# Performance work log

Measured on AMD Instinct MI355X. Metric: run time of the kernel, lower is better.

## Reference

```python
import jax, jax.numpy as jnp
import numpy as np

B, T, D = 32, 1024, 1024
N, L = 256, 768
H = 16
TE = 2048


def layernorm(x, g, b, eps=1e-5):
    m = jnp.mean(x, axis=-1, keepdims=True)
    v = jnp.var(x, axis=-1, keepdims=True)
    return (x - m) * jax.lax.rsqrt(v + eps) * g + b


def setup_inputs() -> dict:
    key = jax.random.key(0)
    ks = jax.random.split(key, 16)
    s = 0.02
    return {
        "x": jax.random.normal(ks[0], (B, T, D), jnp.float32),
        "xf": jax.random.normal(ks[1], (B, N, L), jnp.float32),
        "emb": jax.random.normal(ks[2], (B, TE), jnp.float32),
        "src_mask": jnp.ones((B, T, 1), jnp.float32),
        "cond_type": jax.random.randint(ks[3], (B, 1, 1), 0, 100),
        # LayerNorm params
        "ln_x_g": jnp.ones((D,), jnp.float32), "ln_x_b": jnp.zeros((D,), jnp.float32),
        "ln_t_g": jnp.ones((L,), jnp.float32), "ln_t_b": jnp.zeros((L,), jnp.float32),
        # Q/K/V projections
        "Wq": jax.random.normal(ks[4], (D, D), jnp.float32) * s, "bq": jnp.zeros((D,), jnp.float32),
        "Wk": jax.random.normal(ks[5], (L, D), jnp.float32) * s, "bk": jnp.zeros((D,), jnp.float32),
        "Wv": jax.random.normal(ks[6], (L, D), jnp.float32) * s, "bv": jnp.zeros((D,), jnp.float32),
        # StylizationBlock: SiLU -> Linear(TE, 2D); LayerNorm(D); SiLU -> Linear(D, D)
        "We": jax.random.normal(ks[7], (TE, 2 * D), jnp.float32) * s, "be": jnp.zeros((2 * D,), jnp.float32),
        "ln_y_g": jnp.ones((D,), jnp.float32), "ln_y_b": jnp.zeros((D,), jnp.float32),
        "Wo": jax.random.normal(ks[8], (D, D), jnp.float32) * s, "bo": jnp.zeros((D,), jnp.float32),
    }


def reference(x, xf, emb, src_mask, cond_type,
              ln_x_g, ln_x_b, ln_t_g, ln_t_b,
              Wq, bq, Wk, bk, Wv, bv,
              We, be, ln_y_g, ln_y_b, Wo, bo):
    Bh, Th, Dh = x.shape
    Nn = xf.shape[1]
    head = Dh // H

    # text condition gate: (B,1,1), constant per batch element
    tcond = (cond_type % 10 > 0).astype(x.dtype).reshape(Bh, 1, 1)

    q = (layernorm(x, ln_x_g, ln_x_b) @ Wq + bq).reshape(Bh, Th, H, head)
    xf_n = layernorm(xf, ln_t_g, ln_t_b)
    k = (xf_n @ Wk + bk).reshape(Bh, Nn, H, head)

    # B,T,N,H scores (note: no 1/sqrt(d) scaling, as in the original)
    att = jnp.einsum('bthd,bnhd->btnh', q, k)
    att = att + (1.0 - tcond.reshape(Bh, 1, 1, 1)) * -1000000.0
    att = jax.nn.softmax(att, axis=2)

    v = ((xf_n @ Wv + bv) * tcond).reshape(Bh, Nn, H, head)
    y = jnp.einsum('btnh,bnhd->bthd', att, v).reshape(Bh, Th, Dh)

    # StylizationBlock (dropout inactive in eval)
    emb_out = jax.nn.silu(emb) @ We + be            # B, 2D
    scale, shift = jnp.split(emb_out, 2, axis=-1)   # B, D each
    h = layernorm(y, ln_y_g, ln_y_b) * (1.0 + scale[:, None, :]) + shift[:, None, :]
    h = jax.nn.silu(h) @ Wo + bo
    return x + h
```

## Files before the change

### kernel.cpp

```cpp
#include <hip/hip_runtime.h>
#include <hip/hip_bf16.h>

#define DEV __device__ __forceinline__

typedef __attribute__((ext_vector_type(8))) short bf16x8;
typedef __attribute__((ext_vector_type(4))) float f32x4;
typedef __attribute__((ext_vector_type(8))) unsigned short u16x8;

DEV unsigned short f2bf(float f){
  unsigned int b = __float_as_uint(f);
  return (unsigned short)((b + 0x7fffu + ((b >> 16) & 1u)) >> 16);
}
DEV float bf2f(unsigned short u){ return __uint_as_float(((unsigned int)u)<<16); }

DEV float silu_f(float v){ return v / (1.f + __expf(-v)); }

DEV void gl_lds16(const void* g, void* l){
  __builtin_amdgcn_global_load_lds((const __attribute__((address_space(1))) void*)g,
                                   (__attribute__((address_space(3))) void*)l, 16, 0, 0);
}

__global__ __launch_bounds__(256) void ln_rows(const float* __restrict__ x,
    const float* __restrict__ g, const float* __restrict__ bt,
    unsigned short* __restrict__ out, int D, int nvec)
{
  int row = blockIdx.x, t = threadIdx.x;
  const float4* xr = (const float4*)(x + (size_t)row * D);
  float4 v = make_float4(0.f,0.f,0.f,0.f);
  if (t < nvec) v = xr[t];
  float s  = v.x+v.y+v.z+v.w;
  float s2 = v.x*v.x+v.y*v.y+v.z*v.z+v.w*v.w;
  #pragma unroll
  for (int o=32;o;o>>=1){ s += __shfl_down(s,o,64); s2 += __shfl_down(s2,o,64); }
  __shared__ float red[8];
  if ((t&63)==0){ red[t>>6]=s; red[4+(t>>6)]=s2; }
  __syncthreads();
  float fs  = red[0]+red[1]+red[2]+red[3];
  float fs2 = red[4]+red[5]+red[6]+red[7];
  float mean = fs / (float)D;
  float var  = fmaxf(fs2/(float)D - mean*mean, 0.f);
  float rstd = rsqrtf(var + 1e-5f);
  if (t < nvec){
    float4 gv = ((const float4*)g)[t];
    float4 bv = ((const float4*)bt)[t];
    ushort4 o4;
    o4.x = f2bf((v.x-mean)*rstd*gv.x + bv.x);
    o4.y = f2bf((v.y-mean)*rstd*gv.y + bv.y);
    o4.z = f2bf((v.z-mean)*rstd*gv.z + bv.z);
    o4.w = f2bf((v.w-mean)*rstd*gv.w + bv.w);
    *(ushort4*)(out + (size_t)row*D + t*4) = o4;
  }
}

__global__ __launch_bounds__(256) void wconv(const float* __restrict__ W,
    unsigned short* __restrict__ Wt, int K, int N)
{
  __shared__ float tile[32][33];
  int n0 = blockIdx.x<<5, k0 = blockIdx.y<<5;
  int tx = threadIdx.x & 31, ty = threadIdx.x >> 5;
  #pragma unroll
  for (int i=0;i<4;i++)
    tile[ty + i*8][tx] = W[(size_t)(k0 + ty + i*8)*N + n0 + tx];
  __syncthreads();
  #pragma unroll
  for (int i=0;i<4;i++)
    Wt[(size_t)(n0 + ty + i*8)*K + k0 + tx] = f2bf(tile[tx][ty + i*8]);
}

__global__ __launch_bounds__(256) void bcat(const float* __restrict__ a,
    const float* __restrict__ b, float* __restrict__ o)
{
  int i = blockIdx.x*256 + threadIdx.x;
  o[i] = (i < 1024) ? a[i] : b[i-1024];
}

template<int EPI>
__global__ __launch_bounds__(256,4) void gemm128(
  const unsigned char* __restrict__ A, const unsigned char* __restrict__ Wt,
  const float* __restrict__ bias, void* __restrict__ Cout,
  const float* __restrict__ Xadd, int M, int N, int K, int gxshift)
{
  __shared__ __align__(16) unsigned char lds[32768];
  const int nwg = gridDim.x;
  const int chunk = nwg >> 3;
  const int wg = blockIdx.x;
  const int lg = (wg & 7) * chunk + (wg >> 3);
  const int bx = lg & ((1<<gxshift)-1);
  const int by = lg >> gxshift;
  const int tid = threadIdx.x, w = tid>>6, lane = tid&63;
  const int l15 = lane&15, lq = lane>>4;
  const int m0 = by<<7, n0 = bx<<7;
  const size_t K2 = (size_t)K<<1;
  const int KT = K>>6;
  const int wr = (w>>1)&1, wc = w&1;
  const int srow = lane>>3;
  const int scb  = (lane&7)<<4;

  f32x4 acc[4][4];
  f32x4 zero = {0.f,0.f,0.f,0.f};
  #pragma unroll
  for (int i=0;i<4;i++)
    #pragma unroll
    for (int j=0;j<4;j++) acc[i][j] = zero;

  auto stage = [&](int kt){
    const size_t kb = (size_t)kt<<7;
    #pragma unroll
    for (int inst=0; inst<4; ++inst){
      int base = w*1024 + inst*4096;
      int row  = (base>>7) + srow;
      int cs   = scb ^ ((row&7)<<4);
      gl_lds16(A  + (size_t)(m0+row)*K2 + kb + cs, lds + base);
      gl_lds16(Wt + (size_t)(n0+row)*K2 + kb + cs, lds + 16384 + base);
    }
  };

  for (int kt=0; kt<KT; ++kt){
    stage(kt);
    __syncthreads();
    const unsigned char* ldsA = lds;
    const unsigned char* ldsB = lds + 16384;
    bf16x8 af[2][4], bfr[2][4];
    #pragma unroll
    for (int i=0;i<4;i++){
      int r = wr*64 + i*16 + l15;
      int rb = r<<7, sw = (r&7)<<4;
      af[0][i] = *(const bf16x8*)(ldsA + rb + ((lq*16) ^ sw));
      af[1][i] = *(const bf16x8*)(ldsA + rb + ((64 + lq*16) ^ sw));
    }
    #pragma unroll
    for (int j=0;j<4;j++){
      int r = wc*64 + j*16 + l15;
      int rb = r<<7, sw = (r&7)<<4;
      bfr[0][j] = *(const bf16x8*)(ldsB + rb + ((lq*16) ^ sw));
      bfr[1][j] = *(const bf16x8*)(ldsB + rb + ((64 + lq*16) ^ sw));
    }
    #pragma unroll
    for (int kc=0;kc<2;kc++)
      #pragma unroll
      for (int i=0;i<4;i++)
        #pragma unroll
        for (int j=0;j<4;j++)
          acc[i][j] = __builtin_amdgcn_mfma_f32_16x16x32_bf16(af[kc][i], bfr[kc][j], acc[i][j], 0,0,0);
    __syncthreads();
  }
  #pragma unroll
  for (int j=0;j<4;j++){
    int n = n0 + wc*64 + j*16 + l15;
    float bv = bias[n];
    #pragma unroll
    for (int i=0;i<4;i++){
      int mb = m0 + wr*64 + i*16 + lq*4;
      #pragma unroll
      for (int r=0;r<4;r++){
        size_t idx = (size_t)(mb+r)*N + n;
        float val = acc[i][j][r] + bv;
        if (EPI==0) ((unsigned short*)Cout)[idx] = f2bf(val);
        else        ((float*)Cout)[idx] = Xadd[idx] + val;
      }
    }
  }
}

__global__ __launch_bounds__(256) void vtransp(const unsigned short* __restrict__ v,
                                               int vstride, unsigned char* __restrict__ vt)
{
  __shared__ __align__(16) unsigned short tile[16384];
  int h = blockIdx.x, b = blockIdx.y, tid = threadIdx.x;
  const unsigned short* src = v + (size_t)b*256*vstride + h*64;
  #pragma unroll
  for (int it=0; it<8; ++it){
    int idx = it*256 + tid;
    int n = idx>>3, dc = idx&7;
    *(f32x4*)&tile[n*64 + dc*8] = *(const f32x4*)(src + (size_t)n*vstride + dc*8);
  }
  __syncthreads();
  unsigned char* dst = vt + (size_t)(b*16+h)*32768;
  #pragma unroll
  for (int it=0; it<8; ++it){
    int idx = it*256 + tid;
    int d = idx>>5, nc = idx&31;
    u16x8 o;
    #pragma unroll
    for (int j=0;j<8;j++) o[j] = tile[(nc*8+j)*64 + d];
    *(u16x8*)(dst + d*512 + ((nc*16) ^ ((d&7)<<4))) = o;
  }
}

__global__ __launch_bounds__(256,2) void attn64(
  const unsigned char* __restrict__ qg, const unsigned char* __restrict__ kg,
  int kstride, const unsigned char* __restrict__ vtg, const int* __restrict__ cond,
  unsigned short* __restrict__ yout)
{
  __shared__ __align__(16) unsigned char lds[73728];
  const int wg = blockIdx.x;
  const int lg = (wg & 7) * 1024 + (wg >> 3);
  const int t0 = (lg & 15) * 64;
  const int h  = (lg >> 4) & 15;
  const int b  = lg >> 8;
  const int tid = threadIdx.x, w = tid>>6, lane = tid&63;
  const int l15 = lane&15, lq = lane>>4;

  const unsigned char* kbase = kg + (size_t)b*256*kstride + (size_t)h*128;
  const unsigned char* vtb   = vtg + (size_t)(b*16+h)*32768;
  #pragma unroll
  for (int i=0;i<8;i++){
    int base = (w*8+i)*1024;
    int n  = (base>>7) + (lane>>3);
    int cb = (lane&7)<<4;
    gl_lds16(kbase + (size_t)n*kstride + (cb ^ ((n&7)<<4)), lds + base);
    gl_lds16(vtb + base + lane*16, lds + 32768 + base);
  }
  const unsigned char* qbase = qg + (size_t)(b*1024 + t0)*2048 + h*128;
  #pragma unroll
  for (int i=0;i<2;i++){
    int row = i*32 + (tid>>3);
    int cs  = ((tid&7)<<4) ^ ((row&7)<<4);
    gl_lds16(qbase + (size_t)row*2048 + cs, lds + 65536 + i*4096 + w*1024);
  }
  __syncthreads();

  const int qr = w*16 + l15;
  const int qsw = (qr&7)<<4;
  bf16x8 aq0 = *(const bf16x8*)(lds + 65536 + qr*128 + ((lq*16) ^ qsw));
  bf16x8 aq1 = *(const bf16x8*)(lds + 65536 + qr*128 + ((64 + lq*16) ^ qsw));

  f32x4 zero = {0.f,0.f,0.f,0.f};
  f32x4 s[16];
  #pragma unroll
  for (int nt=0;nt<16;nt++) s[nt] = zero;
  #pragma unroll
  for (int nt=0;nt<16;nt++){
    int n = nt*16 + l15;
    int rb = n<<7, sw = (n&7)<<4;
    bf16x8 kb0 = *(const bf16x8*)(lds + rb + ((lq*16) ^ sw));
    bf16x8 kb1 = *(const bf16x8*)(lds + rb + ((64 + lq*16) ^ sw));
    s[nt] = __builtin_amdgcn_mfma_f32_16x16x32_bf16(aq0, kb0, s[nt], 0,0,0);
    s[nt] = __builtin_amdgcn_mfma_f32_16x16x32_bf16(aq1, kb1, s[nt], 0,0,0);
  }
  #pragma unroll
  for (int r=0;r<4;r++){
    float m = s[0][r];
    #pragma unroll
    for (int nt=1;nt<16;nt++) m = fmaxf(m, s[nt][r]);
    m = fmaxf(m, __shfl_xor(m,1,64));
    m = fmaxf(m, __shfl_xor(m,2,64));
    m = fmaxf(m, __shfl_xor(m,4,64));
    m = fmaxf(m, __shfl_xor(m,8,64));
    float sum = 0.f;
    #pragma unroll
    for (int nt=0;nt<16;nt++){ float p = __expf(s[nt][r]-m); s[nt][r]=p; sum+=p; }
    sum += __shfl_xor(sum,1,64);
    sum += __shfl_xor(sum,2,64);
    sum += __shfl_xor(sum,4,64);
    sum += __shfl_xor(sum,8,64);
    float inv = 1.f/sum;
    #pragma unroll
    for (int nt=0;nt<16;nt++) s[nt][r] *= inv;
  }
  __syncthreads();
  #pragma unroll
  for (int nt=0;nt<16;nt++){
    int n = nt*16 + l15;
    int nb = (n>>3)<<4, nr = (n&7)<<1;
    #pragma unroll
    for (int r=0;r<4;r++){
      int tl = w*16 + lq*4 + r;
      *(unsigned short*)(lds + tl*512 + ((nb ^ ((tl&7)<<4)) | nr)) = f2bf(s[nt][r]);
    }
  }
  __syncthreads();
  f32x4 yv[4];
  #pragma unroll
  for (int dt=0;dt<4;dt++) yv[dt] = zero;
  const int tl = w*16 + l15;
  const int swp = (tl&7)<<4;
  #pragma unroll
  for (int kc=0;kc<8;kc++){
    bf16x8 pa = *(const bf16x8*)(lds + tl*512 + ((kc*64 + lq*16) ^ swp));
    #pragma unroll
    for (int dt=0;dt<4;dt++){
      int d = dt*16 + l15;
      bf16x8 vbv = *(const bf16x8*)(lds + 32768 + d*512 + ((kc*64 + lq*16) ^ ((d&7)<<4)));
      yv[dt] = __builtin_amdgcn_mfma_f32_16x16x32_bf16(pa, vbv, yv[dt], 0,0,0);
    }
  }
  float tc = (cond[b] % 10 > 0) ? 1.f : 0.f;
  #pragma unroll
  for (int dt=0;dt<4;dt++){
    #pragma unroll
    for (int r=0;r<4;r++){
      int tt = t0 + w*16 + lq*4 + r;
      yout[(size_t)(b*1024 + tt)*1024 + h*64 + dt*16 + l15] = f2bf(yv[dt][r]*tc);
    }
  }
}

__global__ __launch_bounds__(256) void embgemm(const float* __restrict__ emb,
    const float* __restrict__ We, float* __restrict__ epart)
{
  __shared__ float a[32][128];
  int cb = blockIdx.x, ks = blockIdx.y, tid = threadIdx.x;
  int k0 = ks<<7;
  #pragma unroll
  for (int it=0; it<4; ++it){
    int fi = it*256 + tid;
    int r = fi>>5, c4 = (fi&31)<<2;
    float4 vv = *(const float4*)(emb + (size_t)r*2048 + k0 + c4);
    vv.x = silu_f(vv.x); vv.y = silu_f(vv.y); vv.z = silu_f(vv.z); vv.w = silu_f(vv.w);
    *(float4*)&a[r][c4] = vv;
  }
  __syncthreads();
  int c0 = (cb<<8) + tid;
  float acc[32];
  #pragma unroll
  for (int r=0;r<32;r++) acc[r]=0.f;
  for (int kk=0;kk<128;kk++){
    float wv = We[(size_t)(k0+kk)*2048 + c0];
    #pragma unroll
    for (int r=0;r<32;r++) acc[r] += a[r][kk]*wv;
  }
  #pragma unroll
  for (int r=0;r<32;r++) epart[(size_t)(ks*32 + r)*2048 + c0] = acc[r];
}

__global__ __launch_bounds__(256) void embred(const float* __restrict__ epart,
    const float* __restrict__ be, float* __restrict__ eo)
{
  int idx = blockIdx.x*256 + threadIdx.x;
  float s = be[idx & 2047];
  #pragma unroll
  for (int ks=0;ks<16;ks++) s += epart[(size_t)ks*65536 + idx];
  eo[idx] = s;
}

__global__ __launch_bounds__(256) void styl(const unsigned short* __restrict__ y,
    const float* __restrict__ g, const float* __restrict__ bt,
    const float* __restrict__ eo, unsigned short* __restrict__ hout)
{
  int row = blockIdx.x, t = threadIdx.x, b = row>>10;
  ushort4 yv4 = ((const ushort4*)(y + (size_t)row*1024))[t];
  float in[4] = {bf2f(yv4.x), bf2f(yv4.y), bf2f(yv4.z), bf2f(yv4.w)};
  float s  = in[0]+in[1]+in[2]+in[3];
  float s2 = in[0]*in[0]+in[1]*in[1]+in[2]*in[2]+in[3]*in[3];
  #pragma unroll
  for (int o=32;o;o>>=1){ s += __shfl_down(s,o,64); s2 += __shfl_down(s2,o,64); }
  __shared__ float red[8];
  if ((t&63)==0){ red[t>>6]=s; red[4+(t>>6)]=s2; }
  __syncthreads();
  float fs  = red[0]+red[1]+red[2]+red[3];
  float fs2 = red[4]+red[5]+red[6]+red[7];
  float mean = fs*(1.f/1024.f);
  float var  = fmaxf(fs2*(1.f/1024.f) - mean*mean, 0.f);
  float rstd = rsqrtf(var + 1e-5f);
  float4 gv = ((const float4*)g)[t];
  float4 bv = ((const float4*)bt)[t];
  float4 sc = ((const float4*)(eo + (size_t)b*2048))[t];
  float4 sh = ((const float4*)(eo + (size_t)b*2048 + 1024))[t];
  float gg[4]  = {gv.x,gv.y,gv.z,gv.w};
  float bb[4]  = {bv.x,bv.y,bv.z,bv.w};
  float scs[4] = {sc.x,sc.y,sc.z,sc.w};
  float shs[4] = {sh.x,sh.y,sh.z,sh.w};
  unsigned short oo[4];
  #pragma unroll
  for (int c=0;c<4;c++){
    float hv = (in[c]-mean)*rstd*gg[c] + bb[c];
    hv = hv*(1.f+scs[c]) + shs[c];
    oo[c] = f2bf(silu_f(hv));
  }
  ushort4 o4; o4.x=oo[0]; o4.y=oo[1]; o4.z=oo[2]; o4.w=oo[3];
  *(ushort4*)(hout + (size_t)row*1024 + t*4) = o4;
}

extern "C" void kernel_launch(void* const* d_in, const int* in_sizes, int n_in,
                              void* d_out, int out_size, void* d_ws, size_t ws_size,
                              hipStream_t stream) {
  const float* x      = (const float*)d_in[0];
  const float* xf     = (const float*)d_in[1];
  const float* emb    = (const float*)d_in[2];
  const int*   cond   = (const int*)d_in[4];
  const float* ln_x_g = (const float*)d_in[5];
  const float* ln_x_b = (const float*)d_in[6];
  const float* ln_t_g = (const float*)d_in[7];
  const float* ln_t_b = (const float*)d_in[8];
  const float* Wq     = (const float*)d_in[9];
  const float* bq     = (const float*)d_in[10];
  const float* Wk     = (const float*)d_in[11];
  const float* bk     = (const float*)d_in[12];
  const float* Wv     = (const float*)d_in[13];
  const float* bv     = (const float*)d_in[14];
  const float* We     = (const float*)d_in[15];
  const float* be     = (const float*)d_in[16];
  const float* ln_y_g = (const float*)d_in[17];
  const float* ln_y_b = (const float*)d_in[18];
  const float* Wo     = (const float*)d_in[19];
  const float* bo     = (const float*)d_in[20];
  float* out = (float*)d_out;

  unsigned char* ws = (unsigned char*)d_ws;
  size_t off = 0;
  auto take = [&](size_t n){ unsigned char* p = ws + off; off += (n + 255) & ~(size_t)255; return p; };
  unsigned char* r1   = take(67108864);
  unsigned char* qb   = take(67108864);
  unsigned char* xfn  = take(12582912);
  unsigned char* kvb  = take(33554432);
  unsigned char* vtb  = take(16777216);
  unsigned char* wqt  = take(2097152);
  unsigned char* wkvt = take(3145728);
  unsigned char* wot  = take(2097152);
  unsigned char* eo   = take(262144);
  unsigned char* bkv  = take(8192);
  float* epart = (float*)r1;

  dim3 blk(256);
  wconv<<<dim3(32,32), blk, 0, stream>>>(Wq, (unsigned short*)wqt, 1024, 1024);
  wconv<<<dim3(32,24), blk, 0, stream>>>(Wk, (unsigned short*)wkvt,  768, 1024);
  wconv<<<dim3(32,24), blk, 0, stream>>>(Wv, (unsigned short*)wkvt + (size_t)1024*768, 768, 1024);
  wconv<<<dim3(32,32), blk, 0, stream>>>(Wo, (unsigned short*)wot, 1024, 1024);
  bcat<<<8, blk, 0, stream>>>(bk, bv, (float*)bkv);
  ln_rows<<<32768, blk, 0, stream>>>(x,  ln_x_g, ln_x_b, (unsigned short*)r1,  1024, 256);
  ln_rows<<<8192,  blk, 0, stream>>>(xf, ln_t_g, ln_t_b, (unsigned short*)xfn,  768, 192);
  gemm128<0><<<2048, blk, 0, stream>>>(r1,  wqt,  bq, qb, nullptr, 32768, 1024, 1024, 3);
  gemm128<0><<<1024, blk, 0, stream>>>(xfn, wkvt, (const float*)bkv, kvb, nullptr, 8192, 2048, 768, 4);
  vtransp<<<dim3(16,32), blk, 0, stream>>>((const unsigned short*)kvb + 1024, 2048, vtb);
  embgemm<<<dim3(8,16), blk, 0, stream>>>(emb, We, epart);
  embred<<<256, blk, 0, stream>>>(epart, be, (float*)eo);
  attn64<<<8192, blk, 0, stream>>>(qb, kvb, 4096, vtb, cond, (unsigned short*)qb);
  styl<<<32768, blk, 0, stream>>>((const unsigned short*)qb, ln_y_g, ln_y_b, (const float*)eo, (unsigned short*)r1);
  gemm128<1><<<2048, blk, 0, stream>>>(r1, wot, bo, out, x, 32768, 1024, 1024, 3);
}
```

Baseline: 487.0 us.

## Replace 128x128 GEMM with 256x256 double-buffered, phase-interleaved 8-wave GEMM

Replaces the 128x128 single-buffered GEMM with a 256x256 tile kernel using 512 threads and two 64KB LDS buffers. Global-to-LDS loads for the next two k-steps are issued between four MFMA phases, with barriers and setprio around each phase. The goal is to hide global load latency and raise arithmetic intensity per LDS byte for the Q, KV and output projections. The cost is 128KB of LDS per block, which limits occupancy. The hand-tuned vmcnt waits are fragile and must match the order of the issued loads.

```diff
diff --git a/kernel.cpp b/kernel.cpp
--- a/kernel.cpp
+++ b/kernel.cpp
@@ -74,13 +74,26 @@
   o[i] = (i < 1024) ? a[i] : b[i-1024];
 }
 
+template<int MH, int KS>
+DEV void phase_mfma(f32x4 (&acc)[8][4], const bf16x8 (&aF)[4], const bf16x8 (&bB)[2][4]){
+  __builtin_amdgcn_s_barrier();
+  __builtin_amdgcn_s_setprio(1);
+  #pragma unroll
+  for (int i=0;i<4;i++)
+    #pragma unroll
+    for (int j=0;j<4;j++)
+      acc[MH*4+i][j] = __builtin_amdgcn_mfma_f32_16x16x32_bf16(aF[i], bB[KS][j], acc[MH*4+i][j], 0,0,0);
+  __builtin_amdgcn_s_setprio(0);
+  __builtin_amdgcn_s_barrier();
+}
+
 template<int EPI>
-__global__ __launch_bounds__(256,4) void gemm128(
+__global__ __launch_bounds__(512,2) void gemm256(
   const unsigned char* __restrict__ A, const unsigned char* __restrict__ Wt,
   const float* __restrict__ bias, void* __restrict__ Cout,
   const float* __restrict__ Xadd, int M, int N, int K, int gxshift)
 {
-  __shared__ __align__(16) unsigned char lds[32768];
+  __shared__ __align__(16) unsigned char lds[131072];
   const int nwg = gridDim.x;
   const int chunk = nwg >> 3;
   const int wg = blockIdx.x;
@@ -89,72 +102,85 @@
   const int by = lg >> gxshift;
   const int tid = threadIdx.x, w = tid>>6, lane = tid&63;
   const int l15 = lane&15, lq = lane>>4;
-  const int m0 = by<<7, n0 = bx<<7;
+  const int wr = w>>2, wc = w&3;
+  const int m0 = by<<8, n0 = bx<<8;
   const size_t K2 = (size_t)K<<1;
-  const int KT = K>>6;
-  const int wr = (w>>1)&1, wc = w&1;
-  const int srow = lane>>3;
-  const int scb  = (lane&7)<<4;
-
-  f32x4 acc[4][4];
+  const int NT = K>>6;
+
+  const int srow = w*8 + (lane>>3);
+  const int scs  = (((lane&7) ^ (lane>>3))<<4);
+
+  f32x4 acc[8][4];
   f32x4 zero = {0.f,0.f,0.f,0.f};
   #pragma unroll
-  for (int i=0;i<4;i++)
+  for (int i=0;i<8;i++)
     #pragma unroll
     for (int j=0;j<4;j++) acc[i][j] = zero;
 
-  auto stage = [&](int kt){
-    const size_t kb = (size_t)kt<<7;
-    #pragma unroll
-    for (int inst=0; inst<4; ++inst){
-      int base = w*1024 + inst*4096;
-      int row  = (base>>7) + srow;
-      int cs   = scb ^ ((row&7)<<4);
-      gl_lds16(A  + (size_t)(m0+row)*K2 + kb + cs, lds + base);
-      gl_lds16(Wt + (size_t)(n0+row)*K2 + kb + cs, lds + 16384 + base);
-    }
+  auto stg = [&](int bf, int mat, int c, int t){
+    const unsigned char* src = mat ? Wt : A;
+    int prow = mat ? n0 : m0;
+    gl_lds16(src + (size_t)(prow + c*64 + srow)*K2 + ((size_t)t<<7) + scs,
+             lds + bf*65536 + mat*32768 + c*8192 + w*1024);
   };
-
-  for (int kt=0; kt<KT; ++kt){
-    stage(kt);
-    __syncthreads();
-    const unsigned char* ldsA = lds;
-    const unsigned char* ldsB = lds + 16384;
-    bf16x8 af[2][4], bfr[2][4];
-    #pragma unroll
-    for (int i=0;i<4;i++){
-      int r = wr*64 + i*16 + l15;
-      int rb = r<<7, sw = (r&7)<<4;
-      af[0][i] = *(const bf16x8*)(ldsA + rb + ((lq*16) ^ sw));
-      af[1][i] = *(const bf16x8*)(ldsA + rb + ((64 + lq*16) ^ sw));
-    }
-    #pragma unroll
-    for (int j=0;j<4;j++){
-      int r = wc*64 + j*16 + l15;
-      int rb = r<<7, sw = (r&7)<<4;
-      bfr[0][j] = *(const bf16x8*)(ldsB + rb + ((lq*16) ^ sw));
-      bfr[1][j] = *(const bf16x8*)(ldsB + rb + ((64 + lq*16) ^ sw));
-    }
-    #pragma unroll
-    for (int kc=0;kc<2;kc++)
-      #pragma unroll
-      for (int i=0;i<4;i++)
-        #pragma unroll
-        for (int j=0;j<4;j++)
-          acc[i][j] = __builtin_amdgcn_mfma_f32_16x16x32_bf16(af[kc][i], bfr[kc][j], acc[i][j], 0,0,0);
-    __syncthreads();
-  }
+  auto ldA = [&](int mh, int i, int ks, int bf)->bf16x8 {
+    int r = wr*128 + mh*64 + i*16 + l15;
+    return *(const bf16x8*)(lds + bf*65536 + r*128 + ((ks*64 + lq*16) ^ ((r&7)<<4)));
+  };
+  auto ldB = [&](int j, int ks, int bf)->bf16x8 {
+    int r = wc*64 + j*16 + l15;
+    return *(const bf16x8*)(lds + bf*65536 + 32768 + r*128 + ((ks*64 + lq*16) ^ ((r&7)<<4)));
+  };
+
+  stg(0,0,0,0); stg(0,0,2,0);
+  stg(0,1,0,0); stg(0,1,1,0);
+  stg(0,1,2,0); stg(0,1,3,0);
+  stg(0,0,1,0); stg(0,0,3,0);
+  stg(1,0,0,1); stg(1,0,2,1);
+  stg(1,1,0,1); stg(1,1,1,1);
+
+  for (int u=0; u<NT; ++u){
+    const int buf = u&1, nb = buf^1;
+    if (u+1 < NT) { asm volatile("s_waitcnt vmcnt(4)" ::: "memory"); }
+    else          { asm volatile("s_waitcnt vmcnt(0)" ::: "memory"); }
+    __builtin_amdgcn_sched_barrier(0);
+    __builtin_amdgcn_s_barrier();
+
+    bf16x8 bB[2][4];
+    bf16x8 aF[4];
+    #pragma unroll
+    for (int j=0;j<4;j++) bB[0][j] = ldB(j,0,buf);
+    #pragma unroll
+    for (int i=0;i<4;i++) aF[i] = ldA(0,i,0,buf);
+    if (u+1 < NT){ stg(nb,1,2,u+1); stg(nb,1,3,u+1); }
+    phase_mfma<0,0>(acc, aF, bB);
+    #pragma unroll
+    for (int j=0;j<4;j++) bB[1][j] = ldB(j,1,buf);
+    #pragma unroll
+    for (int i=0;i<4;i++) aF[i] = ldA(0,i,1,buf);
+    if (u+1 < NT){ stg(nb,0,1,u+1); stg(nb,0,3,u+1); }
+    phase_mfma<0,1>(acc, aF, bB);
+    #pragma unroll
+    for (int i=0;i<4;i++) aF[i] = ldA(1,i,0,buf);
+    if (u+2 < NT){ stg(buf,0,0,u+2); stg(buf,0,2,u+2); }
+    phase_mfma<1,0>(acc, aF, bB);
+    #pragma unroll
+    for (int i=0;i<4;i++) aF[i] = ldA(1,i,1,buf);
+    if (u+2 < NT){ stg(buf,1,0,u+2); stg(buf,1,1,u+2); }
+    phase_mfma<1,1>(acc, aF, bB);
+  }
+
   #pragma unroll
   for (int j=0;j<4;j++){
     int n = n0 + wc*64 + j*16 + l15;
     float bv = bias[n];
     #pragma unroll
-    for (int i=0;i<4;i++){
-      int mb = m0 + wr*64 + i*16 + lq*4;
+    for (int mf=0;mf<8;mf++){
+      int mb = m0 + wr*128 + mf*16 + lq*4;
       #pragma unroll
       for (int r=0;r<4;r++){
         size_t idx = (size_t)(mb+r)*N + n;
-        float val = acc[i][j][r] + bv;
+        float val = acc[mf][j][r] + bv;
         if (EPI==0) ((unsigned short*)Cout)[idx] = f2bf(val);
         else        ((float*)Cout)[idx] = Xadd[idx] + val;
       }
@@ -413,6 +439,7 @@
   float* epart = (float*)r1;
 
   dim3 blk(256);
+  dim3 blk512(512);
   wconv<<<dim3(32,32), blk, 0, stream>>>(Wq, (unsigned short*)wqt, 1024, 1024);
   wconv<<<dim3(32,24), blk, 0, stream>>>(Wk, (unsigned short*)wkvt,  768, 1024);
   wconv<<<dim3(32,24), blk, 0, stream>>>(Wv, (unsigned short*)wkvt + (size_t)1024*768, 768, 1024);
@@ -420,12 +447,12 @@
   bcat<<<8, blk, 0, stream>>>(bk, bv, (float*)bkv);
   ln_rows<<<32768, blk, 0, stream>>>(x,  ln_x_g, ln_x_b, (unsigned short*)r1,  1024, 256);
   ln_rows<<<8192,  blk, 0, stream>>>(xf, ln_t_g, ln_t_b, (unsigned short*)xfn,  768, 192);
-  gemm128<0><<<2048, blk, 0, stream>>>(r1,  wqt,  bq, qb, nullptr, 32768, 1024, 1024, 3);
-  gemm128<0><<<1024, blk, 0, stream>>>(xfn, wkvt, (const float*)bkv, kvb, nullptr, 8192, 2048, 768, 4);
+  gemm256<0><<<512, blk512, 0, stream>>>(r1,  wqt,  bq, qb, nullptr, 32768, 1024, 1024, 2);
+  gemm256<0><<<256, blk512, 0, stream>>>(xfn, wkvt, (const float*)bkv, kvb, nullptr, 8192, 2048, 768, 3);
   vtransp<<<dim3(16,32), blk, 0, stream>>>((const unsigned short*)kvb + 1024, 2048, vtb);
   embgemm<<<dim3(8,16), blk, 0, stream>>>(emb, We, epart);
   embred<<<256, blk, 0, stream>>>(epart, be, (float*)eo);
   attn64<<<8192, blk, 0, stream>>>(qb, kvb, 4096, vtb, cond, (unsigned short*)qb);
   styl<<<32768, blk, 0, stream>>>((const unsigned short*)qb, ln_y_g, ln_y_b, (const float*)eo, (unsigned short*)r1);
-  gemm128<1><<<2048, blk, 0, stream>>>(r1, wot, bo, out, x, 32768, 1024, 1024, 3);
-}
+  gemm256<1><<<512, blk512, 0, stream>>>(r1, wot, bo, out, x, 32768, 1024, 1024, 2);
+}
```

Measured after the change: 495.8 us. Within noise of the previous version (+1.8%).
